# Kernel optimization log

Measured on AMD Instinct MI355X. Metric: run time of the kernel, lower is better.

## Reference

```python
import jax, jax.numpy as jnp
import numpy as np

B, D_IN, H, E, V, L = 2048, 512, 512, 512, 1024, 32
TEMP = 1.0


def setup_inputs() -> dict:
    key = jax.random.key(0)
    ks = jax.random.split(key, 12)
    s = lambda k, shape, scale: jax.random.normal(k, shape, jnp.float32) * scale
    u = jax.random.uniform(ks[11], (L, B, V), jnp.float32, 1e-10, 1.0 - 1e-10)
    gumbel = -jnp.log(-jnp.log(u))
    return {
        'x': s(ks[0], (B, D_IN), 1.0),
        'W_agent': s(ks[1], (D_IN, H), 1.0 / np.sqrt(D_IN)),
        'b_agent': jnp.zeros((H,), jnp.float32),
        'W_ih': s(ks[2], (3 * H, E), 1.0 / np.sqrt(E)),
        'W_hh': s(ks[3], (3 * H, H), 1.0 / np.sqrt(H)),
        'b_ih': jnp.zeros((3 * H,), jnp.float32),
        'b_hh': jnp.zeros((3 * H,), jnp.float32),
        'W_out': s(ks[4], (H, V), 1.0 / np.sqrt(H)),
        'b_out': jnp.zeros((V,), jnp.float32),
        'W_emb': s(ks[5], (V, E), 1.0 / np.sqrt(V)),
        'b_emb': jnp.zeros((E,), jnp.float32),
        'sos': s(ks[6], (E,), 0.01),
        'gumbel': gumbel,
    }


def reference(x, W_agent, b_agent, W_ih, W_hh, b_ih, b_hh, W_out, b_out,
              W_emb, b_emb, sos, gumbel):
    # agent: initial hidden state [B, H]
    h0 = x @ W_agent + b_agent
    e0 = jnp.broadcast_to(sos, (x.shape[0], E))

    def step(carry, g_t):
        h, e = carry
        gx = e @ W_ih.T + b_ih            # [B, 3H]
        gh = h @ W_hh.T + b_hh            # [B, 3H]
        xr, xz, xn = jnp.split(gx, 3, axis=-1)
        hr, hz, hn = jnp.split(gh, 3, axis=-1)
        r = jax.nn.sigmoid(xr + hr)
        z = jax.nn.sigmoid(xz + hz)
        n = jnp.tanh(xn + r * hn)
        h_new = (1.0 - z) * n + z * h     # GRU update
        logits = h_new @ W_out + b_out    # [B, V]
        # RelaxedOneHotCategorical rsample == softmax((logits + gumbel)/T)
        sample = jax.nn.softmax((logits + g_t) / TEMP, axis=-1)
        e_new = sample @ W_emb + b_emb    # [B, E]
        return (h_new, e_new), sample

    _, seq = jax.lax.scan(step, (h0, e0), gumbel)   # [L, B, V]
    seq = jnp.transpose(seq, (1, 0, 2))             # [B, L, V]
    eos = jnp.zeros((seq.shape[0], 1, V), seq.dtype).at[:, 0, 0].set(1.0)
    return jnp.concatenate([seq, eos], axis=1)      # [B, L+1, V]
```

## Files before the change

### kernel.cpp

```cpp
#include <hip/hip_runtime.h>
#include <math.h>

#define B_   2048
#define DIN_ 512
#define H_   512
#define E_   512
#define V_   1024
#define L_   32
#define OUTLD (33 * 1024)

typedef unsigned short u16;
typedef __attribute__((ext_vector_type(8))) __bf16 bf16x8;
typedef __attribute__((ext_vector_type(4))) float f32x4;

__device__ __forceinline__ u16 f2bf(float f) {
    unsigned u = __float_as_uint(f);
    return (u16)((u + 0x7fffu + ((u >> 16) & 1u)) >> 16);
}

__device__ __forceinline__ void gload16(const u16* g, u16* l) {
    __builtin_amdgcn_global_load_lds(
        (const __attribute__((address_space(1))) void*)g,
        (__attribute__((address_space(3))) void*)l, 16, 0, 0);
}

__global__ __launch_bounds__(256) void cvt4_k(const float* __restrict__ s,
                                              u16* __restrict__ d) {
    const int i = (blockIdx.x * 256 + threadIdx.x) * 4;
    const float4 v = *(const float4*)(s + i);
    *(ushort4*)(d + i) = make_ushort4(f2bf(v.x), f2bf(v.y), f2bf(v.z), f2bf(v.w));
}

__global__ __launch_bounds__(256) void cvtT_k(const float* __restrict__ src,
                                              u16* __restrict__ dst, int R, int C) {
    __shared__ float t[32][33];
    const int bc = blockIdx.x * 32, br = blockIdx.y * 32;
    const int tx = threadIdx.x & 31, ty = threadIdx.x >> 5;
    #pragma unroll
    for (int i = 0; i < 32; i += 8)
        t[ty + i][tx] = src[(long)(br + ty + i) * C + bc + tx];
    __syncthreads();
    #pragma unroll
    for (int i = 0; i < 32; i += 8)
        dst[(long)(bc + ty + i) * R + br + tx] = f2bf(t[tx][ty + i]);
}

template<int BM, int BN, bool WF32, bool WBF16>
__device__ __forceinline__ void gemm_body(const u16* __restrict__ A, int lda,
                                          const u16* __restrict__ Bm, int ldb,
                                          const float* __restrict__ bias,
                                          float* __restrict__ C, long ldc,
                                          u16* __restrict__ Cb, int ldcb, int K) {
    constexpr int MR = BM / 32, NR = BN / 32;
    __shared__ __align__(16) u16 As[BM][32];
    __shared__ __align__(16) u16 Bs[BN][32];
    const int tid = threadIdx.x;
    const int w = tid >> 6, l = tid & 63;
    const int wr = w >> 1, wc = w & 1;
    const int bm = blockIdx.y * BM, bn = blockIdx.x * BN;
    const int srow = l >> 2;
    const int skoff = (l & 3) * 8;

    f32x4 zero = {0.f, 0.f, 0.f, 0.f};
    f32x4 acc[MR][NR];
    #pragma unroll
    for (int i = 0; i < MR; ++i)
        #pragma unroll
        for (int j = 0; j < NR; ++j) acc[i][j] = zero;

    const u16* Abase = A + (long)bm * lda + skoff;
    const u16* Bbase = Bm + (long)bn * ldb + skoff;

    for (int k0 = 0; k0 < K; k0 += 32) {
        __syncthreads();
        #pragma unroll
        for (int i = 0; i < BM / 64; ++i) {
            const int r = w * (BM / 4) + i * 16;
            gload16(Abase + (long)(r + srow) * lda + k0, &As[r][0]);
        }
        #pragma unroll
        for (int i = 0; i < BN / 64; ++i) {
            const int r = w * (BN / 4) + i * 16;
            gload16(Bbase + (long)(r + srow) * ldb + k0, &Bs[r][0]);
        }
        __syncthreads();

        bf16x8 af[MR], bfr[NR];
        #pragma unroll
        for (int mi = 0; mi < MR; ++mi)
            af[mi] = *(const bf16x8*)&As[wr * (BM / 2) + mi * 16 + (l & 15)][(l >> 4) * 8];
        #pragma unroll
        for (int ni = 0; ni < NR; ++ni)
            bfr[ni] = *(const bf16x8*)&Bs[wc * (BN / 2) + ni * 16 + (l & 15)][(l >> 4) * 8];
        #pragma unroll
        for (int mi = 0; mi < MR; ++mi)
            #pragma unroll
            for (int ni = 0; ni < NR; ++ni)
                acc[mi][ni] = __builtin_amdgcn_mfma_f32_16x16x32_bf16(
                    af[mi], bfr[ni], acc[mi][ni], 0, 0, 0);
    }

    #pragma unroll
    for (int mi = 0; mi < MR; ++mi) {
        const int row0 = bm + wr * (BM / 2) + mi * 16 + (l >> 4) * 4;
        #pragma unroll
        for (int ni = 0; ni < NR; ++ni) {
            const int col = bn + wc * (BN / 2) + ni * 16 + (l & 15);
            const float bb = bias[col];
            #pragma unroll
            for (int r = 0; r < 4; ++r) {
                const float v = acc[mi][ni][r] + bb;
                if constexpr (WF32) C[(long)(row0 + r) * ldc + col] = v;
                if constexpr (WBF16) Cb[(long)(row0 + r) * ldcb + col] = f2bf(v);
            }
        }
    }
}

template<int BM, int BN, bool WF32, bool WBF16>
__global__ __launch_bounds__(256) void gemm_k(const u16* __restrict__ A, int lda,
                                              const u16* __restrict__ Bm, int ldb,
                                              const float* __restrict__ bias,
                                              float* __restrict__ C, long ldc,
                                              u16* __restrict__ Cb, int ldcb, int K) {
    gemm_body<BM, BN, WF32, WBF16>(A, lda, Bm, ldb, bias, C, ldc, Cb, ldcb, K);
}

__global__ __launch_bounds__(256) void gemm_dual_k(const u16* __restrict__ e_b,
                                                   const u16* __restrict__ h_b,
                                                   const u16* __restrict__ Wih,
                                                   const u16* __restrict__ Whh,
                                                   const float* __restrict__ b_ih,
                                                   const float* __restrict__ b_hh,
                                                   float* __restrict__ gx,
                                                   float* __restrict__ gh) {
    const bool z = blockIdx.z != 0;
    gemm_body<128, 128, true, false>(z ? h_b : e_b, H_, z ? Whh : Wih, H_,
                                     z ? b_hh : b_ih, z ? gh : gx, 3 * H_,
                                     (u16*)nullptr, 0, H_);
}

__global__ __launch_bounds__(256) void gru_pw(const float* __restrict__ gx,
                                              const float* __restrict__ gh,
                                              float* __restrict__ h,
                                              u16* __restrict__ hb) {
    const int i4 = (blockIdx.x * 256 + threadIdx.x) * 4;
    const int b = i4 >> 9, j = i4 & 511;
    const float* gxr = gx + (long)b * 1536 + j;
    const float* ghr = gh + (long)b * 1536 + j;
    const float4 xr = *(const float4*)gxr;
    const float4 xz = *(const float4*)(gxr + 512);
    const float4 xn = *(const float4*)(gxr + 1024);
    const float4 hr = *(const float4*)ghr;
    const float4 hz = *(const float4*)(ghr + 512);
    const float4 hn = *(const float4*)(ghr + 1024);
    float4 hv = *(const float4*)(h + i4);
#define GRU1(c) { \
        const float r_ = 1.f / (1.f + __expf(-(xr.c + hr.c))); \
        const float z_ = 1.f / (1.f + __expf(-(xz.c + hz.c))); \
        const float t_ = xn.c + r_ * hn.c; \
        const float n_ = 1.f - 2.f / (__expf(2.f * t_) + 1.f); \
        hv.c = (1.f - z_) * n_ + z_ * hv.c; }
    GRU1(x) GRU1(y) GRU1(z) GRU1(w)
#undef GRU1
    *(float4*)(h + i4) = hv;
    *(ushort4*)(hb + i4) = make_ushort4(f2bf(hv.x), f2bf(hv.y), f2bf(hv.z), f2bf(hv.w));
}

__global__ __launch_bounds__(256) void softmax_k(float* __restrict__ base,
                                                 const float* __restrict__ gum,
                                                 u16* __restrict__ sb) {
    __shared__ float red[4];
    const int b = blockIdx.x;
    float* p = base + (long)b * OUTLD;
    const float* g = gum + (long)b * V_;
    const int tid = threadIdx.x;
    const float4 lv = *(const float4*)(p + tid * 4);
    const float4 gv = *(const float4*)(g + tid * 4);
    const float x0 = lv.x + gv.x, x1 = lv.y + gv.y;
    const float x2 = lv.z + gv.z, x3 = lv.w + gv.w;
    float m = fmaxf(fmaxf(x0, x1), fmaxf(x2, x3));
    #pragma unroll
    for (int o = 32; o; o >>= 1) m = fmaxf(m, __shfl_xor(m, o));
    if ((tid & 63) == 0) red[tid >> 6] = m;
    __syncthreads();
    m = fmaxf(fmaxf(red[0], red[1]), fmaxf(red[2], red[3]));
    __syncthreads();
    const float e0 = __expf(x0 - m), e1 = __expf(x1 - m);
    const float e2 = __expf(x2 - m), e3 = __expf(x3 - m);
    float s = e0 + e1 + e2 + e3;
    #pragma unroll
    for (int o = 32; o; o >>= 1) s += __shfl_xor(s, o);
    if ((tid & 63) == 0) red[tid >> 6] = s;
    __syncthreads();
    s = red[0] + red[1] + red[2] + red[3];
    const float inv = 1.0f / s;
    float4 r;
    r.x = e0 * inv; r.y = e1 * inv; r.z = e2 * inv; r.w = e3 * inv;
    *(float4*)(p + tid * 4) = r;
    *(ushort4*)(sb + (long)b * V_ + tid * 4) =
        make_ushort4(f2bf(r.x), f2bf(r.y), f2bf(r.z), f2bf(r.w));
}

__global__ __launch_bounds__(256) void init_e_b(u16* __restrict__ eb,
                                                const float* __restrict__ sos) {
    const int idx = blockIdx.x * 256 + threadIdx.x;
    eb[idx] = f2bf(sos[idx & (E_ - 1)]);
}

__global__ __launch_bounds__(256) void eos_k(float* __restrict__ out) {
    const int idx = blockIdx.x * 256 + threadIdx.x;
    const int b = idx >> 10;
    const int v = idx & (V_ - 1);
    out[((long)b * (L_ + 1) + L_) * V_ + v] = (v == 0) ? 1.0f : 0.0f;
}

extern "C" void kernel_launch(void* const* d_in, const int* in_sizes, int n_in,
                              void* d_out, int out_size, void* d_ws, size_t ws_size,
                              hipStream_t stream) {
    const float* x       = (const float*)d_in[0];
    const float* W_agent = (const float*)d_in[1];
    const float* b_agent = (const float*)d_in[2];
    const float* W_ih    = (const float*)d_in[3];
    const float* W_hh    = (const float*)d_in[4];
    const float* b_ih    = (const float*)d_in[5];
    const float* b_hh    = (const float*)d_in[6];
    const float* W_out   = (const float*)d_in[7];
    const float* b_out   = (const float*)d_in[8];
    const float* W_emb   = (const float*)d_in[9];
    const float* b_emb   = (const float*)d_in[10];
    const float* sos     = (const float*)d_in[11];
    const float* gumbel  = (const float*)d_in[12];
    float* out = (float*)d_out;

    u16* WagT_b  = (u16*)d_ws;
    u16* Wih_b   = WagT_b  + H_ * DIN_;
    u16* Whh_b   = Wih_b   + 3 * H_ * E_;
    u16* WoutT_b = Whh_b   + 3 * H_ * H_;
    u16* WembT_b = WoutT_b + V_ * H_;
    u16* x_b     = WembT_b + E_ * V_;
    u16* h_b     = x_b     + (long)B_ * DIN_;
    u16* e_b     = h_b     + (long)B_ * H_;
    u16* samp_b  = e_b     + (long)B_ * E_;
    float* h     = (float*)(samp_b + (long)B_ * V_);
    float* gx    = h  + (long)B_ * H_;
    float* gh    = gx + (long)B_ * 3 * H_;

    cvtT_k<<<dim3(H_ / 32, DIN_ / 32), 256, 0, stream>>>(W_agent, WagT_b, DIN_, H_);
    cvt4_k<<<(3 * H_ * E_) / 1024, 256, 0, stream>>>(W_ih, Wih_b);
    cvt4_k<<<(3 * H_ * H_) / 1024, 256, 0, stream>>>(W_hh, Whh_b);
    cvtT_k<<<dim3(V_ / 32, H_ / 32), 256, 0, stream>>>(W_out, WoutT_b, H_, V_);
    cvtT_k<<<dim3(E_ / 32, V_ / 32), 256, 0, stream>>>(W_emb, WembT_b, V_, E_);
    cvt4_k<<<((long)B_ * DIN_) / 1024, 256, 0, stream>>>(x, x_b);

    gemm_k<64, 64, true, true><<<dim3(H_ / 64, B_ / 64), 256, 0, stream>>>(
        x_b, DIN_, WagT_b, DIN_, b_agent, h, H_, h_b, H_, DIN_);
    init_e_b<<<(B_ * E_) / 256, 256, 0, stream>>>(e_b, sos);
    eos_k<<<(B_ * V_) / 256, 256, 0, stream>>>(out);

    for (int t = 0; t < L_; ++t) {
        gemm_dual_k<<<dim3(3 * H_ / 128, B_ / 128, 2), 256, 0, stream>>>(
            e_b, h_b, Wih_b, Whh_b, b_ih, b_hh, gx, gh);
        gru_pw<<<((long)B_ * H_) / 1024, 256, 0, stream>>>(gx, gh, h, h_b);
        float* lg = out + (long)t * V_;
        gemm_k<128, 64, true, false><<<dim3(V_ / 64, B_ / 128), 256, 0, stream>>>(
            h_b, H_, WoutT_b, H_, b_out, lg, OUTLD, (u16*)nullptr, 0, H_);
        softmax_k<<<B_, 256, 0, stream>>>(lg, gumbel + (long)t * B_ * V_, samp_b);
        gemm_k<64, 64, false, true><<<dim3(E_ / 64, B_ / 64), 256, 0, stream>>>(
            samp_b, V_, WembT_b, V_, b_emb, (float*)nullptr, 0, e_b, E_, V_);
    }
}
```

Baseline: 2.190 ms.

## Fuse GRU gate GEMMs with pointwise update and double-buffer GEMM LDS tiles

Replaces the dual gate GEMM plus separate GRU pointwise kernel with one kernel. Each block computes all six gate slices for 32 hidden columns from a pre-packed combined weight layout and applies the GRU update in registers, so the B×3H gx/gh intermediates are never written to or read from global memory. Hidden state is ping-ponged between two buffers, because blocks read the old h while others write the new h. The generic GEMM also gains double-buffered LDS staging so the next k-tile loads overlap MFMA work, at the cost of twice the shared memory and a larger per-block tile in the fused kernel.

```diff
diff --git a/kernel.cpp b/kernel.cpp
--- a/kernel.cpp
+++ b/kernel.cpp
@@ -45,6 +45,22 @@
         dst[(long)(bc + ty + i) * R + br + tx] = f2bf(t[tx][ty + i]);
 }
 
+__global__ __launch_bounds__(256) void pack_w_k(const float* __restrict__ Wih,
+                                                const float* __restrict__ Whh,
+                                                u16* __restrict__ dst) {
+    const long idx = ((long)blockIdx.x * 256 + threadIdx.x) * 4;
+    const int k = (int)(idx & 511);
+    const int rowid = (int)(idx >> 9);
+    const int gr = rowid % 192;
+    const int t = rowid / 192;
+    const int g = gr >> 5, r = gr & 31;
+    const float* src = (g < 3)
+        ? Wih + ((long)(g * H_ + t * 32 + r) << 9)
+        : Whh + ((long)((g - 3) * H_ + t * 32 + r) << 9);
+    const float4 v = *(const float4*)(src + k);
+    *(ushort4*)(dst + idx) = make_ushort4(f2bf(v.x), f2bf(v.y), f2bf(v.z), f2bf(v.w));
+}
+
 template<int BM, int BN, bool WF32, bool WBF16>
 __device__ __forceinline__ void gemm_body(const u16* __restrict__ A, int lda,
                                           const u16* __restrict__ Bm, int ldb,
@@ -52,8 +68,8 @@
                                           float* __restrict__ C, long ldc,
                                           u16* __restrict__ Cb, int ldcb, int K) {
     constexpr int MR = BM / 32, NR = BN / 32;
-    __shared__ __align__(16) u16 As[BM][32];
-    __shared__ __align__(16) u16 Bs[BN][32];
+    __shared__ __align__(16) u16 As[2][BM][32];
+    __shared__ __align__(16) u16 Bs[2][BN][32];
     const int tid = threadIdx.x;
     const int w = tid >> 6, l = tid & 63;
     const int wr = w >> 1, wc = w & 1;
@@ -61,44 +77,53 @@
     const int srow = l >> 2;
     const int skoff = (l & 3) * 8;
 
-    f32x4 zero = {0.f, 0.f, 0.f, 0.f};
     f32x4 acc[MR][NR];
     #pragma unroll
     for (int i = 0; i < MR; ++i)
         #pragma unroll
-        for (int j = 0; j < NR; ++j) acc[i][j] = zero;
+        for (int j = 0; j < NR; ++j) acc[i][j] = {0.f, 0.f, 0.f, 0.f};
 
     const u16* Abase = A + (long)bm * lda + skoff;
     const u16* Bbase = Bm + (long)bn * ldb + skoff;
 
-    for (int k0 = 0; k0 < K; k0 += 32) {
-        __syncthreads();
+    auto stage = [&](int buf, int k0) {
         #pragma unroll
         for (int i = 0; i < BM / 64; ++i) {
             const int r = w * (BM / 4) + i * 16;
-            gload16(Abase + (long)(r + srow) * lda + k0, &As[r][0]);
+            gload16(Abase + (long)(r + srow) * lda + k0, &As[buf][r][0]);
         }
         #pragma unroll
         for (int i = 0; i < BN / 64; ++i) {
             const int r = w * (BN / 4) + i * 16;
-            gload16(Bbase + (long)(r + srow) * ldb + k0, &Bs[r][0]);
-        }
-        __syncthreads();
-
+            gload16(Bbase + (long)(r + srow) * ldb + k0, &Bs[buf][r][0]);
+        }
+    };
+    auto compute = [&](int buf) {
         bf16x8 af[MR], bfr[NR];
         #pragma unroll
         for (int mi = 0; mi < MR; ++mi)
-            af[mi] = *(const bf16x8*)&As[wr * (BM / 2) + mi * 16 + (l & 15)][(l >> 4) * 8];
+            af[mi] = *(const bf16x8*)&As[buf][wr * (BM / 2) + mi * 16 + (l & 15)][(l >> 4) * 8];
         #pragma unroll
         for (int ni = 0; ni < NR; ++ni)
-            bfr[ni] = *(const bf16x8*)&Bs[wc * (BN / 2) + ni * 16 + (l & 15)][(l >> 4) * 8];
+            bfr[ni] = *(const bf16x8*)&Bs[buf][wc * (BN / 2) + ni * 16 + (l & 15)][(l >> 4) * 8];
         #pragma unroll
         for (int mi = 0; mi < MR; ++mi)
             #pragma unroll
             for (int ni = 0; ni < NR; ++ni)
                 acc[mi][ni] = __builtin_amdgcn_mfma_f32_16x16x32_bf16(
                     af[mi], bfr[ni], acc[mi][ni], 0, 0, 0);
-    }
+    };
+
+    stage(0, 0);
+    __syncthreads();
+    int cur = 0;
+    for (int k0 = 32; k0 < K; k0 += 32) {
+        stage(cur ^ 1, k0);
+        compute(cur);
+        __syncthreads();
+        cur ^= 1;
+    }
+    compute(cur);
 
     #pragma unroll
     for (int mi = 0; mi < MR; ++mi) {
@@ -126,45 +151,94 @@
     gemm_body<BM, BN, WF32, WBF16>(A, lda, Bm, ldb, bias, C, ldc, Cb, ldcb, K);
 }
 
-__global__ __launch_bounds__(256) void gemm_dual_k(const u16* __restrict__ e_b,
-                                                   const u16* __restrict__ h_b,
-                                                   const u16* __restrict__ Wih,
-                                                   const u16* __restrict__ Whh,
-                                                   const float* __restrict__ b_ih,
-                                                   const float* __restrict__ b_hh,
-                                                   float* __restrict__ gx,
-                                                   float* __restrict__ gh) {
-    const bool z = blockIdx.z != 0;
-    gemm_body<128, 128, true, false>(z ? h_b : e_b, H_, z ? Whh : Wih, H_,
-                                     z ? b_hh : b_ih, z ? gh : gx, 3 * H_,
-                                     (u16*)nullptr, 0, H_);
-}
-
-__global__ __launch_bounds__(256) void gru_pw(const float* __restrict__ gx,
-                                              const float* __restrict__ gh,
-                                              float* __restrict__ h,
-                                              u16* __restrict__ hb) {
-    const int i4 = (blockIdx.x * 256 + threadIdx.x) * 4;
-    const int b = i4 >> 9, j = i4 & 511;
-    const float* gxr = gx + (long)b * 1536 + j;
-    const float* ghr = gh + (long)b * 1536 + j;
-    const float4 xr = *(const float4*)gxr;
-    const float4 xz = *(const float4*)(gxr + 512);
-    const float4 xn = *(const float4*)(gxr + 1024);
-    const float4 hr = *(const float4*)ghr;
-    const float4 hz = *(const float4*)(ghr + 512);
-    const float4 hn = *(const float4*)(ghr + 1024);
-    float4 hv = *(const float4*)(h + i4);
-#define GRU1(c) { \
-        const float r_ = 1.f / (1.f + __expf(-(xr.c + hr.c))); \
-        const float z_ = 1.f / (1.f + __expf(-(xz.c + hz.c))); \
-        const float t_ = xn.c + r_ * hn.c; \
-        const float n_ = 1.f - 2.f / (__expf(2.f * t_) + 1.f); \
-        hv.c = (1.f - z_) * n_ + z_ * hv.c; }
-    GRU1(x) GRU1(y) GRU1(z) GRU1(w)
-#undef GRU1
-    *(float4*)(h + i4) = hv;
-    *(ushort4*)(hb + i4) = make_ushort4(f2bf(hv.x), f2bf(hv.y), f2bf(hv.z), f2bf(hv.w));
+__global__ __launch_bounds__(256) void gru_gemm_k(
+    const u16* __restrict__ e_b,
+    const u16* __restrict__ hb_in,
+    const float* __restrict__ h_in,
+    const u16* __restrict__ Wcomb,
+    const float* __restrict__ b_ih, const float* __restrict__ b_hh,
+    float* __restrict__ h_out, u16* __restrict__ hb_out) {
+    __shared__ __align__(16) u16 lds[2][320][32];
+    const int tid = threadIdx.x;
+    const int w = tid >> 6, l = tid & 63;
+    const int wr = w >> 1, wc = w & 1;
+    const int bn = blockIdx.x * 32;
+    const int bm = blockIdx.y * 64;
+    const int srow = l >> 2;
+    const int skoff = (l & 3) * 8;
+    const u16* WT = Wcomb + (long)blockIdx.x * 192 * 512;
+
+    f32x4 ax[3][2], ah[3][2];
+    #pragma unroll
+    for (int g = 0; g < 3; ++g)
+        #pragma unroll
+        for (int mi = 0; mi < 2; ++mi) {
+            ax[g][mi] = {0.f, 0.f, 0.f, 0.f};
+            ah[g][mi] = {0.f, 0.f, 0.f, 0.f};
+        }
+
+    auto stage = [&](int buf, int k0) {
+        #pragma unroll
+        for (int i = 0; i < 5; ++i) {
+            const int c = w * 5 + i;
+            const u16* src;
+            if (c < 4)      src = e_b   + (long)(bm + c * 16 + srow) * 512;
+            else if (c < 8) src = hb_in + (long)(bm + (c - 4) * 16 + srow) * 512;
+            else            src = WT    + (long)((c - 8) * 16 + srow) * 512;
+            gload16(src + k0 + skoff, &lds[buf][c * 16][0]);
+        }
+    };
+    auto compute = [&](int buf) {
+        bf16x8 ae[2], ahf[2], bf[6];
+        #pragma unroll
+        for (int mi = 0; mi < 2; ++mi) {
+            ae[mi]  = *(const bf16x8*)&lds[buf][wr * 32 + mi * 16 + (l & 15)][(l >> 4) * 8];
+            ahf[mi] = *(const bf16x8*)&lds[buf][64 + wr * 32 + mi * 16 + (l & 15)][(l >> 4) * 8];
+        }
+        #pragma unroll
+        for (int g = 0; g < 6; ++g)
+            bf[g] = *(const bf16x8*)&lds[buf][128 + g * 32 + wc * 16 + (l & 15)][(l >> 4) * 8];
+        #pragma unroll
+        for (int g = 0; g < 3; ++g)
+            #pragma unroll
+            for (int mi = 0; mi < 2; ++mi) {
+                ax[g][mi] = __builtin_amdgcn_mfma_f32_16x16x32_bf16(ae[mi],  bf[g],     ax[g][mi], 0, 0, 0);
+                ah[g][mi] = __builtin_amdgcn_mfma_f32_16x16x32_bf16(ahf[mi], bf[3 + g], ah[g][mi], 0, 0, 0);
+            }
+    };
+
+    stage(0, 0);
+    __syncthreads();
+    int cur = 0;
+    for (int k0 = 32; k0 < 512; k0 += 32) {
+        stage(cur ^ 1, k0);
+        compute(cur);
+        __syncthreads();
+        cur ^= 1;
+    }
+    compute(cur);
+
+    const int col = bn + wc * 16 + (l & 15);
+    const float bxr = b_ih[col], bxz = b_ih[512 + col], bxn = b_ih[1024 + col];
+    const float bhr = b_hh[col], bhz = b_hh[512 + col], bhn = b_hh[1024 + col];
+    #pragma unroll
+    for (int mi = 0; mi < 2; ++mi) {
+        const int row0 = bm + wr * 32 + mi * 16 + (l >> 4) * 4;
+        #pragma unroll
+        for (int r = 0; r < 4; ++r) {
+            const long off = (long)(row0 + r) * 512 + col;
+            const float xr = ax[0][mi][r] + bxr, hr = ah[0][mi][r] + bhr;
+            const float xz = ax[1][mi][r] + bxz, hz = ah[1][mi][r] + bhz;
+            const float xn = ax[2][mi][r] + bxn, hn = ah[2][mi][r] + bhn;
+            const float r_ = 1.f / (1.f + __expf(-(xr + hr)));
+            const float z_ = 1.f / (1.f + __expf(-(xz + hz)));
+            const float t_ = xn + r_ * hn;
+            const float n_ = 1.f - 2.f / (__expf(2.f * t_) + 1.f);
+            const float hv = (1.f - z_) * n_ + z_ * h_in[off];
+            h_out[off] = hv;
+            hb_out[off] = f2bf(hv);
+        }
+    }
 }
 
 __global__ __launch_bounds__(256) void softmax_k(float* __restrict__ base,
@@ -234,37 +308,39 @@
     float* out = (float*)d_out;
 
     u16* WagT_b  = (u16*)d_ws;
-    u16* Wih_b   = WagT_b  + H_ * DIN_;
-    u16* Whh_b   = Wih_b   + 3 * H_ * E_;
-    u16* WoutT_b = Whh_b   + 3 * H_ * H_;
+    u16* Wcomb   = WagT_b  + H_ * DIN_;
+    u16* WoutT_b = Wcomb   + 16 * 192 * 512;
     u16* WembT_b = WoutT_b + V_ * H_;
     u16* x_b     = WembT_b + E_ * V_;
-    u16* h_b     = x_b     + (long)B_ * DIN_;
-    u16* e_b     = h_b     + (long)B_ * H_;
+    u16* hb0     = x_b     + (long)B_ * DIN_;
+    u16* hb1     = hb0     + (long)B_ * H_;
+    u16* e_b     = hb1     + (long)B_ * H_;
     u16* samp_b  = e_b     + (long)B_ * E_;
-    float* h     = (float*)(samp_b + (long)B_ * V_);
-    float* gx    = h  + (long)B_ * H_;
-    float* gh    = gx + (long)B_ * 3 * H_;
+    float* h0    = (float*)(samp_b + (long)B_ * V_);
+    float* h1    = h0 + (long)B_ * H_;
 
     cvtT_k<<<dim3(H_ / 32, DIN_ / 32), 256, 0, stream>>>(W_agent, WagT_b, DIN_, H_);
-    cvt4_k<<<(3 * H_ * E_) / 1024, 256, 0, stream>>>(W_ih, Wih_b);
-    cvt4_k<<<(3 * H_ * H_) / 1024, 256, 0, stream>>>(W_hh, Whh_b);
+    pack_w_k<<<(16 * 192 * 512) / 1024, 256, 0, stream>>>(W_ih, W_hh, Wcomb);
     cvtT_k<<<dim3(V_ / 32, H_ / 32), 256, 0, stream>>>(W_out, WoutT_b, H_, V_);
     cvtT_k<<<dim3(E_ / 32, V_ / 32), 256, 0, stream>>>(W_emb, WembT_b, V_, E_);
     cvt4_k<<<((long)B_ * DIN_) / 1024, 256, 0, stream>>>(x, x_b);
 
     gemm_k<64, 64, true, true><<<dim3(H_ / 64, B_ / 64), 256, 0, stream>>>(
-        x_b, DIN_, WagT_b, DIN_, b_agent, h, H_, h_b, H_, DIN_);
+        x_b, DIN_, WagT_b, DIN_, b_agent, h0, H_, hb0, H_, DIN_);
     init_e_b<<<(B_ * E_) / 256, 256, 0, stream>>>(e_b, sos);
     eos_k<<<(B_ * V_) / 256, 256, 0, stream>>>(out);
 
     for (int t = 0; t < L_; ++t) {
-        gemm_dual_k<<<dim3(3 * H_ / 128, B_ / 128, 2), 256, 0, stream>>>(
-            e_b, h_b, Wih_b, Whh_b, b_ih, b_hh, gx, gh);
-        gru_pw<<<((long)B_ * H_) / 1024, 256, 0, stream>>>(gx, gh, h, h_b);
+        const bool even = (t & 1) == 0;
+        const u16* hbi = even ? hb0 : hb1;
+        u16* hbo       = even ? hb1 : hb0;
+        const float* hi = even ? h0 : h1;
+        float* ho       = even ? h1 : h0;
+        gru_gemm_k<<<dim3(H_ / 32, B_ / 64), 256, 0, stream>>>(
+            e_b, hbi, hi, Wcomb, b_ih, b_hh, ho, hbo);
         float* lg = out + (long)t * V_;
         gemm_k<128, 64, true, false><<<dim3(V_ / 64, B_ / 128), 256, 0, stream>>>(
-            h_b, H_, WoutT_b, H_, b_out, lg, OUTLD, (u16*)nullptr, 0, H_);
+            hbo, H_, WoutT_b, H_, b_out, lg, OUTLD, (u16*)nullptr, 0, H_);
         softmax_k<<<B_, 256, 0, stream>>>(lg, gumbel + (long)t * B_ * V_, samp_b);
         gemm_k<64, 64, false, true><<<dim3(E_ / 64, B_ / 64), 256, 0, stream>>>(
             samp_b, V_, WembT_b, V_, b_emb, (float*)nullptr, 0, e_b, E_, V_);
```

Result: faster. 1.892 ms (-13.6%).
